# Kernel optimization log

Measured on AMD Instinct MI355X. Metric: run time of the kernel, lower is better.

Reference implementation:

```python
import jax, jax.numpy as jnp
import numpy as np
from jax import lax

BN_EPS = 1e-5


def _spatial_gate(x, w, g, b, m, v):
    # x: [N, C, H, W]; ChannelPool -> [N, 2, H, W]; 7x7 conv -> [N,1,H,W]; BN (eval); sigmoid gate
    comp = jnp.stack([jnp.max(x, axis=1), jnp.mean(x, axis=1)], axis=1)
    o = lax.conv_general_dilated(comp, w, (1, 1), [(3, 3), (3, 3)],
                                 dimension_numbers=('NCHW', 'OIHW', 'NCHW'))
    o = (o - m[None, :, None, None]) * lax.rsqrt(v + BN_EPS)[None, :, None, None] \
        * g[None, :, None, None] + b[None, :, None, None]
    s = jax.nn.sigmoid(o)
    return x * s


def _eca_sort(x, w_eca):
    # global avg pool -> sort channels desc -> 1D conv over sorted seq -> sigmoid -> unsort -> gate
    y = jnp.mean(x, axis=(2, 3))               # [N, C]
    order = jnp.argsort(-y, axis=1)            # descending sort indices
    rank = jnp.argsort(order, axis=1)          # inverse permutation
    ys = jnp.take_along_axis(y, order, axis=1)  # sorted descending
    k = w_eca.shape[-1]
    p = k // 2
    o = lax.conv_general_dilated(ys[:, None, :], w_eca, (1,), [(p, p)],
                                 dimension_numbers=('NCH', 'OIH', 'NCH'))[:, 0, :]
    sig = jax.nn.sigmoid(o)
    yr = jnp.take_along_axis(sig, rank, axis=1)  # reorder back per original index_select(rank)
    return x * yr[:, :, None, None]


def setup_inputs() -> dict:
    key = jax.random.key(0)
    ks = jax.random.split(key, 6)
    N, C, H, W = 32, 256, 56, 56
    inp = {
        'x': jax.random.normal(ks[0], (N, C, H, W), dtype=jnp.float32),
        'weight': jax.random.normal(ks[1], (1,), dtype=jnp.float32),
        'w_h': jax.random.normal(ks[2], (1, 2, 7, 7), dtype=jnp.float32) * 0.1,
        'g_h': jnp.ones((1,), jnp.float32), 'b_h': jnp.zeros((1,), jnp.float32),
        'm_h': jnp.zeros((1,), jnp.float32), 'v_h': jnp.ones((1,), jnp.float32),
        'w_w': jax.random.normal(ks[3], (1, 2, 7, 7), dtype=jnp.float32) * 0.1,
        'g_w': jnp.ones((1,), jnp.float32), 'b_w': jnp.zeros((1,), jnp.float32),
        'm_w': jnp.zeros((1,), jnp.float32), 'v_w': jnp.ones((1,), jnp.float32),
        'w_s': jax.random.normal(ks[4], (1, 2, 7, 7), dtype=jnp.float32) * 0.1,
        'g_s': jnp.ones((1,), jnp.float32), 'b_s': jnp.zeros((1,), jnp.float32),
        'm_s': jnp.zeros((1,), jnp.float32), 'v_s': jnp.ones((1,), jnp.float32),
        'w_eca': jax.random.normal(ks[5], (1, 1, 5), dtype=jnp.float32) * 0.3,
    }
    return inp


def reference(x, weight, w_h, g_h, b_h, m_h, v_h, w_w, g_w, b_w, m_w, v_w,
              w_s, g_s, b_s, m_s, v_s, w_eca):
    # branch 1: gate over H-as-channel (permute 0,2,1,3)
    xh = jnp.transpose(x, (0, 2, 1, 3))
    x11 = jnp.transpose(_spatial_gate(xh, w_h, g_h, b_h, m_h, v_h), (0, 2, 1, 3))
    # branch 2: gate over W-as-channel (permute 0,3,2,1)
    xw = jnp.transpose(x, (0, 3, 2, 1))
    x21 = jnp.transpose(_spatial_gate(xw, w_w, g_w, b_w, m_w, v_w), (0, 3, 2, 1))
    # branch 3: eca with sort/unsort
    x31 = _eca_sort(x, w_eca)
    # branch 4: plain spatial gate
    xo = _spatial_gate(x, w_s, g_s, b_s, m_s, v_s)
    return 0.23779 * xo + 0.24695 * x11 + 0.24365 * x21 + 0.27173 * x31
```

## Files before the change

### kernel.cpp

```cpp
#include <hip/hip_runtime.h>
#include <math.h>

#define N_ 32
#define C_ 256
#define H_ 56
#define W_ 56
#define HW_ (H_*W_)
#define HW4_ (HW_/4)
#define CHW_ (C_*HW_)
#define NHW_ (N_*HW_)
#define NHW4_ (NHW_/4)
#define NCW_ (N_*C_*W_)
#define NHC_ (N_*H_*C_)
#define BN_EPS_ 1e-5f

#define TLD 60
#define PPB 16
#define NB_PL 512

#define SM_B(i) ((i) * 3360)
#define SM_CPMX 10080
#define SM_CPSM (10080 + 224)
#define SM_TOT  (10080 + 448)

#define F4MAX(a,b) do { (a).x=fmaxf((a).x,(b).x); (a).y=fmaxf((a).y,(b).y); \
                        (a).z=fmaxf((a).z,(b).z); (a).w=fmaxf((a).w,(b).w); } while(0)
#define F4ADD(a,b) do { (a).x+=(b).x; (a).y+=(b).y; (a).z+=(b).z; (a).w+=(b).w; } while(0)

__global__ __launch_bounds__(256, 4) void pools_k(
        const float* __restrict__ x,
        float* __restrict__ maxH, float* __restrict__ meanH,
        float* __restrict__ maxWt, float* __restrict__ meanWt,
        float* __restrict__ pmx, float* __restrict__ psm,
        float* __restrict__ y) {
    __shared__ float smem[SM_TOT];
    int b = blockIdx.x;
    int tid = threadIdx.x;
    const float4* x4 = (const float4*)x;
    float* cpmx = smem + SM_CPMX;
    float* cpsm = smem + SM_CPSM;
    int pb0 = b * PPB;
    int row0 = tid / 14,          col0 = (tid % 14) * 4;
    int row1 = (tid + 256) / 14,  col1 = ((tid + 256) % 14) * 4;
    int row2 = (tid + 512) / 14,  col2 = ((tid + 512) % 14) * 4;
    int row3 = (tid + 768) / 14,  col3 = ((tid + 768) % 14) * 4;
    float4 a0, a1, a2, a3;
    float4 b0_, b1_, b2_, b3_;
    float4 amx0, amx1, amx2, amx3, asm0, asm1, asm2, asm3;
    amx0 = amx1 = amx2 = amx3 = make_float4(-INFINITY, -INFINITY, -INFINITY, -INFINITY);
    asm0 = asm1 = asm2 = asm3 = make_float4(0.f, 0.f, 0.f, 0.f);

#define ISSUE(R0,R1,R2,R3, P) { size_t _ba = (size_t)(pb0 + (P)) * HW4_;          \
        R0 = x4[_ba + tid]; R1 = x4[_ba + 256 + tid]; R2 = x4[_ba + 512 + tid];   \
        if (tid < 16) R3 = x4[_ba + 768 + tid]; }
#define FOLD(R0,R1,R2,R3) { F4MAX(amx0,R0); F4ADD(asm0,R0);                       \
        F4MAX(amx1,R1); F4ADD(asm1,R1); F4MAX(amx2,R2); F4ADD(asm2,R2);           \
        if (tid < 16) { F4MAX(amx3,R3); F4ADD(asm3,R3); } }
#define STAGE(BUF, R0,R1,R2,R3) { float* _d = smem + (BUF);                       \
        *(float4*)&_d[row0*TLD+col0] = R0; *(float4*)&_d[row1*TLD+col1] = R1;     \
        *(float4*)&_d[row2*TLD+col2] = R2;                                        \
        if (tid < 16) *(float4*)&_d[row3*TLD+col3] = R3; }

    ISSUE(a0, a1, a2, a3, 0);
    FOLD(a0, a1, a2, a3);
    STAGE(SM_B(0), a0, a1, a2, a3);
    ISSUE(b0_, b1_, b2_, b3_, 1);
    __syncthreads();

#define COMPUTE(K) {                                                              \
        const float* cur = smem + SM_B((K) % 3);                                  \
        int pb = pb0 + (K);                                                       \
        int n = pb >> 8, c = pb & 255;                                            \
        if (tid < 224) {                     \
            int w = tid % 56, hq = tid / 56;                                      \
            const float* base = &cur[(hq * 14) * TLD + w];                        \
            float mx = -INFINITY, sm = 0.f;                                       \
            _Pragma("unroll")                                                     \
            for (int hh = 0; hh < 14; ++hh) {                                     \
                float v = base[hh * TLD];                                         \
                mx = fmaxf(mx, v); sm += v;                                       \
            }                                                                     \
            cpmx[hq * 56 + w] = mx; cpsm[hq * 56 + w] = sm;                       \
        }                                                                         \
        if (tid < 224) {                     \
            int h = tid >> 2, kq = tid & 3;                                       \
            const float* base = &cur[h * TLD + kq * 14];                          \
            float mx = -INFINITY, sm = 0.f;                                       \
            _Pragma("unroll")                                                     \
            for (int kk = 0; kk < 14; ++kk) {                                     \
                float v = base[kk];                                               \
                mx = fmaxf(mx, v); sm += v;                                       \
            }                                                                     \
            mx = fmaxf(mx, __shfl_xor(mx, 1)); sm += __shfl_xor(sm, 1);           \
            mx = fmaxf(mx, __shfl_xor(mx, 2)); sm += __shfl_xor(sm, 2);           \
            if (kq == 0) {                                                        \
                int o = (n * C_ + c) * H_ + h;                                    \
                maxWt[o] = mx; meanWt[o] = sm * (1.f / W_);                       \
            }                                                                     \
        }                                                                         \
        __syncthreads();                                                          \
        float colsum = 0.f;                                                       \
        if (tid < 56) {                                                           \
            float mx = cpmx[tid], sm = cpsm[tid];                                 \
            _Pragma("unroll")                                                     \
            for (int j = 1; j < 4; ++j) {                                         \
                mx = fmaxf(mx, cpmx[j * 56 + tid]);                               \
                sm += cpsm[j * 56 + tid];                                         \
            }                                                                     \
            int o = (n * C_ + c) * W_ + tid;                                      \
            maxH[o] = mx; meanH[o] = sm * (1.f / H_);                             \
            colsum = sm;                                                          \
        }                                                                         \
        if (tid < 64) {                                                           \
            float t = colsum;                                                     \
            _Pragma("unroll")                                                     \
            for (int off = 32; off >= 1; off >>= 1) t += __shfl_xor(t, off);      \
            if (tid == 0) y[n * C_ + c] = t * (1.f / HW_);                        \
        }                                                                         \
    }

    #pragma unroll
    for (int k2 = 0; k2 < PPB / 2; ++k2) {
        const int k = 2 * k2;
        if (k + 2 < PPB) ISSUE(a0, a1, a2, a3, k + 2);
        COMPUTE(k);
        FOLD(b0_, b1_, b2_, b3_);
        STAGE(SM_B((k + 1) % 3), b0_, b1_, b2_, b3_);
        __syncthreads();
        if (k + 3 < PPB) ISSUE(b0_, b1_, b2_, b3_, k + 3);
        COMPUTE(k + 1);
        if (k + 2 < PPB) {
            FOLD(a0, a1, a2, a3);
            STAGE(SM_B((k + 2) % 3), a0, a1, a2, a3);
        }
        __syncthreads();
    }
#undef ISSUE
#undef FOLD
#undef STAGE
#undef COMPUTE
    {
        float4* PM = (float4*)pmx + (size_t)b * HW4_;
        float4* PS = (float4*)psm + (size_t)b * HW4_;
        PM[tid] = amx0;        PS[tid] = asm0;
        PM[tid + 256] = amx1;  PS[tid + 256] = asm1;
        PM[tid + 512] = amx2;  PS[tid + 512] = asm2;
        if (tid < 16) { PM[tid + 768] = amx3; PS[tid + 768] = asm3; }
    }
}

__global__ __launch_bounds__(256, 4) void cpool_final_k(
        const float* __restrict__ pmx, const float* __restrict__ psm,
        float* __restrict__ maxC, float* __restrict__ meanC) {
    __shared__ float4 smx[4][64];
    __shared__ float4 ssm[4][64];
    int bb = blockIdx.x;
    int tid = threadIdx.x;
    int oi = tid & 63, g4 = tid >> 6;
    int t = bb * 64 + oi;
    int n = t / HW4_, hw4 = t - n * HW4_;
    const float4* PM = (const float4*)pmx + (size_t)(n * 16 + g4 * 4) * HW4_ + hw4;
    const float4* PS = (const float4*)psm + (size_t)(n * 16 + g4 * 4) * HW4_ + hw4;
    float4 mx = make_float4(-INFINITY, -INFINITY, -INFINITY, -INFINITY);
    float4 sm = make_float4(0.f, 0.f, 0.f, 0.f);
    #pragma unroll
    for (int g = 0; g < 4; ++g) {
        float4 v = PM[(size_t)g * HW4_];
        float4 s = PS[(size_t)g * HW4_];
        F4MAX(mx, v);
        F4ADD(sm, s);
    }
    smx[g4][oi] = mx;
    ssm[g4][oi] = sm;
    __syncthreads();
    if (tid < 64) {
        float4 m = smx[0][tid];
        #pragma unroll
        for (int j = 1; j < 4; ++j) F4MAX(m, smx[j][tid]);
        ((float4*)maxC)[bb * 64 + tid] = m;
    } else if (tid < 128) {
        int t2 = tid - 64;
        float4 s = ssm[0][t2];
        #pragma unroll
        for (int j = 1; j < 4; ++j) F4ADD(s, ssm[j][t2]);
        s.x *= (1.f / C_); s.y *= (1.f / C_); s.z *= (1.f / C_); s.w *= (1.f / C_);
        ((float4*)meanC)[bb * 64 + t2] = s;
    }
}

template <int R, int Cc, bool TR>
__device__ __forceinline__ void conv7_part(int t, const float* __restrict__ p0,
                                           const float* __restrict__ p1,
                                           const float* __restrict__ wt,
                                           float g, float bb, float m, float v,
                                           float* __restrict__ out) {
    const int per = R * Cc;
    int n = t / per;
    int r2 = t - n * per;
    int i = r2 / Cc, j = r2 - i * Cc;
    const float* b0 = p0 + (size_t)n * per;
    const float* b1 = p1 + (size_t)n * per;
    float acc = 0.f;
    #pragma unroll
    for (int ki = 0; ki < 7; ++ki) {
        int ii = i + ki - 3;
        if (ii < 0 || ii >= R) continue;
        #pragma unroll
        for (int kj = 0; kj < 7; ++kj) {
            int jj = j + kj - 3;
            if (jj < 0 || jj >= Cc) continue;
            int idx = ii * Cc + jj;
            int wi = TR ? (kj * 7 + ki) : (ki * 7 + kj);
            acc += b0[idx] * wt[wi] + b1[idx] * wt[49 + wi];
        }
    }
    float o = (acc - m) * rsqrtf(v + BN_EPS_) * g + bb;
    out[t] = 1.f / (1.f + expf(-o));
}

#define NB_SS (NHW_ / 256)
#define NB_SH (NCW_ / 256)
#define NB_SW (NHC_ / 256)

__global__ __launch_bounds__(256) void conv_eca_k(
        const float* __restrict__ maxC, const float* __restrict__ meanC,
        const float* __restrict__ maxH, const float* __restrict__ meanH,
        const float* __restrict__ maxWt, const float* __restrict__ meanWt,
        const float* __restrict__ w_s, const float* __restrict__ g_s,
        const float* __restrict__ b_s, const float* __restrict__ m_s,
        const float* __restrict__ v_s,
        const float* __restrict__ w_h, const float* __restrict__ g_h,
        const float* __restrict__ b_h, const float* __restrict__ m_h,
        const float* __restrict__ v_h,
        const float* __restrict__ w_w, const float* __restrict__ g_w,
        const float* __restrict__ b_w, const float* __restrict__ m_w,
        const float* __restrict__ v_w,
        const float* __restrict__ y, const float* __restrict__ w_eca,
        float* __restrict__ s_s, float* __restrict__ s_h, float* __restrict__ s_wt,
        float* __restrict__ gate) {
    __shared__ float sv[C_];
    __shared__ int si[C_];
    int b = blockIdx.x;
    int tid = threadIdx.x;
    if (b < NB_SS) {
        conv7_part<H_, W_, false>(b * 256 + tid, maxC, meanC, w_s, g_s[0], b_s[0],
                                  m_s[0], v_s[0], s_s);
    } else if (b < NB_SS + NB_SH) {
        conv7_part<C_, W_, false>((b - NB_SS) * 256 + tid, maxH, meanH, w_h, g_h[0],
                                  b_h[0], m_h[0], v_h[0], s_h);
    } else if (b < NB_SS + NB_SH + NB_SW) {
        conv7_part<C_, H_, true>((b - NB_SS - NB_SH) * 256 + tid, maxWt, meanWt, w_w,
                                 g_w[0], b_w[0], m_w[0], v_w[0], s_wt);
    } else {
        int n = b - (NB_SS + NB_SH + NB_SW);
        sv[tid] = y[n * C_ + tid];
        si[tid] = tid;
        __syncthreads();
        for (int k = 2; k <= C_; k <<= 1) {
            for (int j = k >> 1; j > 0; j >>= 1) {
                int ixj = tid ^ j;
                if (ixj > tid) {
                    float v1 = sv[tid], v2 = sv[ixj];
                    int i1 = si[tid], i2 = si[ixj];
                    bool before = (v1 > v2) || (v1 == v2 && i1 < i2);
                    bool dir = ((tid & k) == 0);
                    if (dir ? !before : before) {
                        sv[tid] = v2; sv[ixj] = v1;
                        si[tid] = i2; si[ixj] = i1;
                    }
                }
                __syncthreads();
            }
        }
        float o = 0.f;
        #pragma unroll
        for (int j = 0; j < 5; ++j) {
            int p = tid + j - 2;
            if (p >= 0 && p < C_) o += sv[p] * w_eca[j];
        }
        gate[n * C_ + si[tid]] = 1.f / (1.f + expf(-o));
    }
}

__global__ __launch_bounds__(256) void apply_k(
        const float* __restrict__ x, const float* __restrict__ s_s,
        const float* __restrict__ s_h, const float* __restrict__ s_wt,
        const float* __restrict__ gate, float* __restrict__ out) {
    int t0 = blockIdx.x * 512 + threadIdx.x;
    #pragma unroll
    for (int r = 0; r < 2; ++r) {
        int t = t0 + r * 256;
        int f = t * 4;
        int n = f / CHW_;
        int rem = f - n * CHW_;
        int c = rem / HW_;
        int hw = rem - c * HW_;
        int h = hw / W_;
        int w = hw - h * W_;
        float4 xv = ((const float4*)x)[t];
        float4 s4 = *(const float4*)(s_s + (size_t)n * HW_ + hw);
        float4 h4 = *(const float4*)(s_h + ((size_t)n * C_ + c) * W_ + w);
        float sw = s_wt[((size_t)n * C_ + c) * H_ + h];
        float ge = gate[n * C_ + c];
        float base = 0.24365f * sw + 0.27173f * ge;
        float4 o;
        o.x = xv.x * (0.23779f * s4.x + 0.24695f * h4.x + base);
        o.y = xv.y * (0.23779f * s4.y + 0.24695f * h4.y + base);
        o.z = xv.z * (0.23779f * s4.z + 0.24695f * h4.z + base);
        o.w = xv.w * (0.23779f * s4.w + 0.24695f * h4.w + base);
        ((float4*)out)[t] = o;
    }
}

extern "C" void kernel_launch(void* const* d_in, const int* in_sizes, int n_in,
                              void* d_out, int out_size, void* d_ws, size_t ws_size,
                              hipStream_t stream) {
    const float* x     = (const float*)d_in[0];
    const float* w_h   = (const float*)d_in[2];
    const float* g_h   = (const float*)d_in[3];
    const float* b_h   = (const float*)d_in[4];
    const float* m_h   = (const float*)d_in[5];
    const float* v_h   = (const float*)d_in[6];
    const float* w_w   = (const float*)d_in[7];
    const float* g_w   = (const float*)d_in[8];
    const float* b_w   = (const float*)d_in[9];
    const float* m_w   = (const float*)d_in[10];
    const float* v_w   = (const float*)d_in[11];
    const float* w_s   = (const float*)d_in[12];
    const float* g_s   = (const float*)d_in[13];
    const float* b_s   = (const float*)d_in[14];
    const float* m_s   = (const float*)d_in[15];
    const float* v_s   = (const float*)d_in[16];
    const float* w_eca = (const float*)d_in[17];
    float* out = (float*)d_out;

    float* ws    = (float*)d_ws;
    float* maxC  = ws;
    float* meanC = maxC  + NHW_;
    float* maxH  = meanC + NHW_;
    float* meanH = maxH  + NCW_;
    float* maxWt = meanH + NCW_;
    float* meanWt= maxWt + NHC_;
    float* s_s   = meanWt+ NHC_;
    float* s_h   = s_s   + NHW_;
    float* s_wt  = s_h   + NCW_;
    float* yv    = s_wt  + NHC_;
    float* gate  = yv    + N_ * C_;
    float* pmx   = gate  + N_ * C_;
    float* psm   = pmx   + (size_t)NB_PL * HW_;

    pools_k<<<NB_PL, 256, 0, stream>>>(x, maxH, meanH, maxWt, meanWt, pmx, psm, yv);

    cpool_final_k<<<NHW4_ / 64, 256, 0, stream>>>(pmx, psm, maxC, meanC);

    int conv_blocks = NB_SS + NB_SH + NB_SW + N_;
    conv_eca_k<<<conv_blocks, 256, 0, stream>>>(maxC, meanC, maxH, meanH, maxWt, meanWt,
                                                w_s, g_s, b_s, m_s, v_s,
                                                w_h, g_h, b_h, m_h, v_h,
                                                w_w, g_w, b_w, m_w, v_w,
                                                yv, w_eca, s_s, s_h, s_wt, gate);

    apply_k<<<(N_ * CHW_ / 4) / 512, 256, 0, stream>>>(x, s_s, s_h, s_wt, gate, out);
}
```

Before: 92.35 us.

## Merge H/W pooling passes, double-buffer planes, halve planes per block

The pooling kernel now computes column and row max/sum in one pass per thread with shuffle reductions, which removes the intermediate shared-memory column partials and one barrier per plane. The global-average value y is written one iteration late through a small shared slot, so only one sync per plane remains. The staging ring drops from triple to double buffering, and each block handles 8 planes instead of 16, doubling the block count. The final channel-pool kernel now reduces 8 partials per output instead of 4, which means more partial-buffer traffic in exchange for more parallelism and less shared memory per block.

```diff
diff --git a/kernel.cpp b/kernel.cpp
--- a/kernel.cpp
+++ b/kernel.cpp
@@ -15,13 +15,12 @@
 #define BN_EPS_ 1e-5f
 
 #define TLD 60
-#define PPB 16
-#define NB_PL 512
-
-#define SM_B(i) ((i) * 3360)
-#define SM_CPMX 10080
-#define SM_CPSM (10080 + 224)
-#define SM_TOT  (10080 + 448)
+#define PPB 8
+#define NB_PL 1024
+
+#define SM_BUF(i) ((i) * 3360)
+#define SM_YS 6720
+#define SM_TOT (6720 + 8)
 
 #define F4MAX(a,b) do { (a).x=fmaxf((a).x,(b).x); (a).y=fmaxf((a).y,(b).y); \
                         (a).z=fmaxf((a).z,(b).z); (a).w=fmaxf((a).w,(b).w); } while(0)
@@ -37,15 +36,15 @@
     int b = blockIdx.x;
     int tid = threadIdx.x;
     const float4* x4 = (const float4*)x;
-    float* cpmx = smem + SM_CPMX;
-    float* cpsm = smem + SM_CPSM;
     int pb0 = b * PPB;
     int row0 = tid / 14,          col0 = (tid % 14) * 4;
     int row1 = (tid + 256) / 14,  col1 = ((tid + 256) % 14) * 4;
     int row2 = (tid + 512) / 14,  col2 = ((tid + 512) % 14) * 4;
     int row3 = (tid + 768) / 14,  col3 = ((tid + 768) % 14) * 4;
-    float4 a0, a1, a2, a3;
-    float4 b0_, b1_, b2_, b3_;
+    int wq = tid >> 2, q4 = tid & 3;
+    bool act = tid < 224;
+    int wvid = tid >> 6;
+    float4 a0, a1, a2, a3, b0_, b1_, b2_, b3_;
     float4 amx0, amx1, amx2, amx3, asm0, asm1, asm2, asm3;
     amx0 = amx1 = amx2 = amx3 = make_float4(-INFINITY, -INFINITY, -INFINITY, -INFINITY);
     asm0 = asm1 = asm2 = asm3 = make_float4(0.f, 0.f, 0.f, 0.f);
@@ -63,82 +62,71 @@
 
     ISSUE(a0, a1, a2, a3, 0);
     FOLD(a0, a1, a2, a3);
-    STAGE(SM_B(0), a0, a1, a2, a3);
+    STAGE(SM_BUF(0), a0, a1, a2, a3);
     ISSUE(b0_, b1_, b2_, b3_, 1);
     __syncthreads();
 
-#define COMPUTE(K) {                                                              \
-        const float* cur = smem + SM_B((K) % 3);                                  \
-        int pb = pb0 + (K);                                                       \
-        int n = pb >> 8, c = pb & 255;                                            \
-        if (tid < 224) {                     \
-            int w = tid % 56, hq = tid / 56;                                      \
-            const float* base = &cur[(hq * 14) * TLD + w];                        \
-            float mx = -INFINITY, sm = 0.f;                                       \
-            _Pragma("unroll")                                                     \
-            for (int hh = 0; hh < 14; ++hh) {                                     \
-                float v = base[hh * TLD];                                         \
-                mx = fmaxf(mx, v); sm += v;                                       \
-            }                                                                     \
-            cpmx[hq * 56 + w] = mx; cpsm[hq * 56 + w] = sm;                       \
-        }                                                                         \
-        if (tid < 224) {                     \
-            int h = tid >> 2, kq = tid & 3;                                       \
-            const float* base = &cur[h * TLD + kq * 14];                          \
-            float mx = -INFINITY, sm = 0.f;                                       \
-            _Pragma("unroll")                                                     \
-            for (int kk = 0; kk < 14; ++kk) {                                     \
-                float v = base[kk];                                               \
-                mx = fmaxf(mx, v); sm += v;                                       \
-            }                                                                     \
-            mx = fmaxf(mx, __shfl_xor(mx, 1)); sm += __shfl_xor(sm, 1);           \
-            mx = fmaxf(mx, __shfl_xor(mx, 2)); sm += __shfl_xor(sm, 2);           \
-            if (kq == 0) {                                                        \
-                int o = (n * C_ + c) * H_ + h;                                    \
-                maxWt[o] = mx; meanWt[o] = sm * (1.f / W_);                       \
-            }                                                                     \
-        }                                                                         \
-        __syncthreads();                                                          \
-        float colsum = 0.f;                                                       \
-        if (tid < 56) {                                                           \
-            float mx = cpmx[tid], sm = cpsm[tid];                                 \
-            _Pragma("unroll")                                                     \
-            for (int j = 1; j < 4; ++j) {                                         \
-                mx = fmaxf(mx, cpmx[j * 56 + tid]);                               \
-                sm += cpsm[j * 56 + tid];                                         \
-            }                                                                     \
-            int o = (n * C_ + c) * W_ + tid;                                      \
-            maxH[o] = mx; meanH[o] = sm * (1.f / H_);                             \
-            colsum = sm;                                                          \
-        }                                                                         \
-        if (tid < 64) {                                                           \
-            float t = colsum;                                                     \
-            _Pragma("unroll")                                                     \
-            for (int off = 32; off >= 1; off >>= 1) t += __shfl_xor(t, off);      \
-            if (tid == 0) y[n * C_ + c] = t * (1.f / HW_);                        \
-        }                                                                         \
-    }
-
     #pragma unroll
-    for (int k2 = 0; k2 < PPB / 2; ++k2) {
-        const int k = 2 * k2;
-        if (k + 2 < PPB) ISSUE(a0, a1, a2, a3, k + 2);
-        COMPUTE(k);
-        FOLD(b0_, b1_, b2_, b3_);
-        STAGE(SM_B((k + 1) % 3), b0_, b1_, b2_, b3_);
+    for (int k = 0; k < PPB; ++k) {
+        if (k + 2 < PPB) {
+            if ((k & 1) == 0) { ISSUE(a0, a1, a2, a3, k + 2); }
+            else              { ISSUE(b0_, b1_, b2_, b3_, k + 2); }
+        }
+        const float* cur = smem + SM_BUF(k & 1);
+        int pb = pb0 + k;
+        int n = pb >> 8, c = pb & 255;
+        float cmx = -INFINITY, csm = 0.f, rmx = -INFINITY, rsm = 0.f;
+        if (act) {
+            const float* cb = &cur[(q4 * 14) * TLD + wq];
+            #pragma unroll
+            for (int hh = 0; hh < 14; ++hh) {
+                float v = cb[hh * TLD];
+                cmx = fmaxf(cmx, v); csm += v;
+            }
+            const float* rb = &cur[wq * TLD + q4 * 14];
+            #pragma unroll
+            for (int kk = 0; kk < 14; ++kk) {
+                float v = rb[kk];
+                rmx = fmaxf(rmx, v); rsm += v;
+            }
+        }
+        cmx = fmaxf(cmx, __shfl_xor(cmx, 1)); csm += __shfl_xor(csm, 1);
+        cmx = fmaxf(cmx, __shfl_xor(cmx, 2)); csm += __shfl_xor(csm, 2);
+        rmx = fmaxf(rmx, __shfl_xor(rmx, 1)); rsm += __shfl_xor(rsm, 1);
+        rmx = fmaxf(rmx, __shfl_xor(rmx, 2)); rsm += __shfl_xor(rsm, 2);
+        if (act && q4 == 0) {
+            int oH = (n * C_ + c) * W_ + wq;
+            maxH[oH] = cmx; meanH[oH] = csm * (1.f / H_);
+            int oW = (n * C_ + c) * H_ + wq;
+            maxWt[oW] = rmx; meanWt[oW] = rsm * (1.f / W_);
+        }
+        float rs = (act && q4 == 0) ? rsm : 0.f;
+        #pragma unroll
+        for (int off = 32; off >= 1; off >>= 1) rs += __shfl_xor(rs, off);
+        if ((tid & 63) == 0) smem[SM_YS + (k & 1) * 4 + wvid] = rs;
+        if (k > 0 && tid == 0) {
+            int s = ((k - 1) & 1) * 4;
+            float t = smem[SM_YS + s] + smem[SM_YS + s + 1] +
+                      smem[SM_YS + s + 2] + smem[SM_YS + s + 3];
+            y[pb - 1] = t * (1.f / HW_);
+        }
+        if (k + 1 < PPB) {
+            if ((k & 1) == 0) { FOLD(b0_, b1_, b2_, b3_);
+                                STAGE(SM_BUF((k + 1) & 1), b0_, b1_, b2_, b3_); }
+            else              { FOLD(a0, a1, a2, a3);
+                                STAGE(SM_BUF((k + 1) & 1), a0, a1, a2, a3); }
+        }
         __syncthreads();
-        if (k + 3 < PPB) ISSUE(b0_, b1_, b2_, b3_, k + 3);
-        COMPUTE(k + 1);
-        if (k + 2 < PPB) {
-            FOLD(a0, a1, a2, a3);
-            STAGE(SM_B((k + 2) % 3), a0, a1, a2, a3);
-        }
-        __syncthreads();
+    }
+    if (tid == 0) {
+        int s = ((PPB - 1) & 1) * 4;
+        float t = smem[SM_YS + s] + smem[SM_YS + s + 1] +
+                  smem[SM_YS + s + 2] + smem[SM_YS + s + 3];
+        y[pb0 + PPB - 1] = t * (1.f / HW_);
     }
 #undef ISSUE
 #undef FOLD
 #undef STAGE
-#undef COMPUTE
     {
         float4* PM = (float4*)pmx + (size_t)b * HW4_;
         float4* PS = (float4*)psm + (size_t)b * HW4_;
@@ -159,12 +147,12 @@
     int oi = tid & 63, g4 = tid >> 6;
     int t = bb * 64 + oi;
     int n = t / HW4_, hw4 = t - n * HW4_;
-    const float4* PM = (const float4*)pmx + (size_t)(n * 16 + g4 * 4) * HW4_ + hw4;
-    const float4* PS = (const float4*)psm + (size_t)(n * 16 + g4 * 4) * HW4_ + hw4;
+    const float4* PM = (const float4*)pmx + (size_t)(n * 32 + g4 * 8) * HW4_ + hw4;
+    const float4* PS = (const float4*)psm + (size_t)(n * 32 + g4 * 8) * HW4_ + hw4;
     float4 mx = make_float4(-INFINITY, -INFINITY, -INFINITY, -INFINITY);
     float4 sm = make_float4(0.f, 0.f, 0.f, 0.f);
     #pragma unroll
-    for (int g = 0; g < 4; ++g) {
+    for (int g = 0; g < 8; ++g) {
         float4 v = PM[(size_t)g * HW4_];
         float4 s = PS[(size_t)g * HW4_];
         F4MAX(mx, v);
```

Measured after the change: 112.1 us. 1.21x slower.
